# Performance work log

Hardware: AMD Instinct MI355X
Metric: run time of the kernel (lower is better)

The kernel has to match this reference:

```python
import jax, jax.numpy as jnp
import numpy as np

N_NODES = 50000
DEG = 16           # constant out-degree per center node
CUTOFF = 5.0


def setup_inputs() -> dict:
    key = jax.random.key(0)
    k1, k2 = jax.random.split(key)
    # positions scaled so a meaningful fraction of edges exceed the cutoff
    pos = jax.random.normal(k1, (N_NODES, 3), dtype=jnp.float32) * 3.0
    row = jnp.repeat(jnp.arange(N_NODES, dtype=jnp.int32), DEG)      # [E]
    col = jax.random.randint(k2, (N_NODES * DEG,), 0, N_NODES, dtype=jnp.int32)
    edge_index = jnp.stack([row, col], axis=0)                        # [2, E]
    return {"pos": pos, "edge_index": edge_index}


def reference(pos, edge_index):
    """Padded, vectorized DimeNet-style triplet generation.

    Assumes constant degree: edge_index[0] == repeat(arange(N), DEG), so the
    neighbor list of node i is edge_index[1].reshape(N, DEG)[i]. Triplets are
    the [N, DEG, DEG] all-pairs grid; `mask` marks entries that the original
    Python-loop implementation would actually emit (both edges within cutoff,
    j-slot != k-slot).  Masked slots carry 0 for angles/distances.
    """
    num_nodes = pos.shape[0]
    deg = edge_index.shape[1] // num_nodes
    nb = edge_index[1].reshape(num_nodes, deg)          # [N, d] neighbor ids

    R1 = pos[nb] - pos[:, None, :]                      # [N, d, 3] i -> neighbor vectors
    edge_dist = jnp.linalg.norm(R1, axis=-1)            # [N, d]
    valid = edge_dist <= CUTOFF                         # cutoff filter per edge

    diag = jnp.eye(deg, dtype=bool)
    mask = valid[:, :, None] & valid[:, None, :] & ~diag  # [N, d, d]

    # angle(j, i, k) = atan2(|R1_j x R1_k|, R1_j . R1_k)
    dot = jnp.einsum('njc,nkc->njk', R1, R1)            # [N, d, d]
    cross = jnp.cross(R1[:, :, None, :], R1[:, None, :, :])  # [N, d, d, 3]
    cn2 = jnp.sum(cross * cross, axis=-1)
    cross_norm = jnp.sqrt(jnp.where(mask, cn2, 1.0))    # safe sqrt on padded slots
    angles = jnp.where(mask, jnp.arctan2(cross_norm, dot), 0.0)

    # |pos_j - pos_k| = |R1_j - R1_k|
    dvec = R1[:, :, None, :] - R1[:, None, :, :]
    d2 = jnp.sum(dvec * dvec, axis=-1)
    distances_jk = jnp.where(mask, jnp.sqrt(jnp.where(mask & (d2 > 0), d2, 1.0)), 0.0)

    shape3 = (num_nodes, deg, deg)
    id3_i = jnp.broadcast_to(jnp.arange(num_nodes, dtype=jnp.int32)[:, None, None], shape3).reshape(-1)
    id3_j = jnp.broadcast_to(nb[:, :, None], shape3).reshape(-1)
    id3_k = jnp.broadcast_to(nb[:, None, :], shape3).reshape(-1)

    return (id3_i, id3_j, id3_k,
            distances_jk.reshape(-1), angles.reshape(-1), mask.reshape(-1))
```

## Files before the change

kernel.cpp:

```cpp
#include <hip/hip_runtime.h>


#define DEG 16
#define NODES_PER_BLOCK 16
#define THREADS (NODES_PER_BLOCK * 64)
#define CUTOFF_F 5.0f

typedef float f32x4 __attribute__((ext_vector_type(4)));

__device__ __forceinline__ float fast_atan2_pos(float y, float x) {
    const float PI_F   = 3.14159274f;
    const float PIO2_F = 1.57079637f;
    const float ax = fabsf(x);
    const float mn = fminf(ax, y);
    const float mx = fmaxf(ax, y);
    const float a = (mx > 0.0f) ? __fdividef(mn, mx) : 0.0f;
    const float s = a * a;
    float r = fmaf(s, fmaf(s, fmaf(s, fmaf(s, 0.0208351f, -0.085133f),
                                   0.180141f), -0.3302995f), 0.9998660f);
    r *= a;
    if (y > ax)    r = PIO2_F - r;
    if (x < 0.0f)  r = PI_F - r;
    return r;
}

__global__ __launch_bounds__(THREADS) void triplet_kernel(
    const float* __restrict__ pos,
    const int* __restrict__ col_idx,
    float* __restrict__ out,
    int num_nodes, int P)
{
    __shared__ float sx[THREADS / 4], sy[THREADS / 4], sz[THREADS / 4];
    __shared__ float scolf[THREADS / 4];
    __shared__ int   sval[THREADS / 4];

    const int base = blockIdx.x * NODES_PER_BLOCK;
    const int tid = threadIdx.x;

    if (tid < NODES_PER_BLOCK * DEG) {
        int nl = tid >> 4;
        int slot = tid & 15;
        int node = base + nl;
        if (node < num_nodes) {
            int c = col_idx[node * DEG + slot];
            float px = pos[3 * node], py = pos[3 * node + 1], pz = pos[3 * node + 2];
            float rx = pos[3 * c]     - px;
            float ry = pos[3 * c + 1] - py;
            float rz = pos[3 * c + 2] - pz;
            float d = sqrtf(rx * rx + ry * ry + rz * rz);
            sx[tid] = rx; sy[tid] = ry; sz[tid] = rz;
            scolf[tid] = (float)c;
            sval[tid] = (d <= CUTOFF_F) ? 1 : 0;
        }
    }
    __syncthreads();

    const int w = tid >> 6;
    const int lane = tid & 63;
    const int node = base + w;
    if (node >= num_nodes) return;

    const int ofs = w * DEG;
    const int j = lane >> 2;
    const int k0 = (lane & 3) << 2;

    const float jx = sx[ofs + j], jy = sy[ofs + j], jz = sz[ofs + j];
    const int   jv = sval[ofs + j];
    const float jcolf = scolf[ofs + j];

    f32x4 o_k, o_d, o_a, o_m;

    #pragma unroll
    for (int q = 0; q < 4; ++q) {
        const int k = k0 + q;
        const float kx = sx[ofs + k], ky = sy[ofs + k], kz = sz[ofs + k];
        const int   kv = sval[ofs + k];
        const bool m = (jv != 0) && (kv != 0) && (j != k);

        const float dot = jx * kx + jy * ky + jz * kz;
        const float cx = jy * kz - jz * ky;
        const float cy = jz * kx - jx * kz;
        const float cz = jx * ky - jy * kx;
        const float cn2 = cx * cx + cy * cy + cz * cz;
        const float ang = m ? fast_atan2_pos(sqrtf(cn2), dot) : 0.0f;

        const float dx = jx - kx, dy = jy - ky, dz = jz - kz;
        const float d2 = dx * dx + dy * dy + dz * dz;
        const float dist = m ? sqrtf(d2 > 0.0f ? d2 : 1.0f) : 0.0f;

        o_k[q] = scolf[ofs + k];
        o_d[q] = dist;
        o_a[q] = ang;
        o_m[q] = m ? 1.0f : 0.0f;
    }

    const int idx = node * (DEG * DEG) + lane * 4;
    const float fi = (float)node;
    f32x4 o_i; o_i[0] = fi; o_i[1] = fi; o_i[2] = fi; o_i[3] = fi;
    f32x4 o_j; o_j[0] = jcolf; o_j[1] = jcolf; o_j[2] = jcolf; o_j[3] = jcolf;

    float* o0 = out + idx;
    *reinterpret_cast<f32x4*>(o0)         = o_i;
    *reinterpret_cast<f32x4*>(o0 + P)     = o_j;
    *reinterpret_cast<f32x4*>(o0 + 2 * P) = o_k;
    *reinterpret_cast<f32x4*>(o0 + 3 * P) = o_d;
    *reinterpret_cast<f32x4*>(o0 + 4 * P) = o_a;
    *reinterpret_cast<f32x4*>(o0 + 5 * P) = o_m;
}

extern "C" void kernel_launch(void* const* d_in, const int* in_sizes, int n_in,
                              void* d_out, int out_size, void* d_ws, size_t ws_size,
                              hipStream_t stream) {
    const float* pos = (const float*)d_in[0];
    const int* edge_index = (const int*)d_in[1];

    const int num_nodes = in_sizes[0] / 3;
    const int E = in_sizes[1] / 2;
    const int* col = edge_index + E;

    const int P = num_nodes * (DEG * DEG);
    const int blocks = (num_nodes + NODES_PER_BLOCK - 1) / NODES_PER_BLOCK;

    triplet_kernel<<<blocks, THREADS, 0, stream>>>(
        pos, col, (float*)d_out, num_nodes, P);
}
```

Measured before the change: 53.34 us.

## Process two node batches per block, prefetching second batch gathers during first compute

Each block now handles two groups of 16 nodes. The column indices and position gathers for the second group are issued before the first group's triplet compute and stores, so their latency can overlap that work. The second group is then staged into its own shared buffer behind a manual waitcnt and barrier. This halves the grid size and adds register and shared-memory pressure, while the kernel stays dominated by its large output writes.

Result: no change. 53.83 us (+0.9%).

```diff
diff --git a/kernel.cpp b/kernel.cpp
--- a/kernel.cpp
+++ b/kernel.cpp
@@ -2,8 +2,8 @@
 
 
 #define DEG 16
-#define NODES_PER_BLOCK 16
-#define THREADS (NODES_PER_BLOCK * 64)
+#define NPB 16
+#define THREADS (NPB * 64)
 #define CUTOFF_F 5.0f
 
 typedef float f32x4 __attribute__((ext_vector_type(4)));
@@ -24,40 +24,13 @@
     return r;
 }
 
-__global__ __launch_bounds__(THREADS) void triplet_kernel(
-    const float* __restrict__ pos,
-    const int* __restrict__ col_idx,
-    float* __restrict__ out,
-    int num_nodes, int P)
+__device__ __forceinline__ void compute_store(
+    const float* __restrict__ sx, const float* __restrict__ sy,
+    const float* __restrict__ sz, const float* __restrict__ scolf,
+    const int* __restrict__ sval,
+    int node, int num_nodes, int w, int lane,
+    float* __restrict__ out, int P)
 {
-    __shared__ float sx[THREADS / 4], sy[THREADS / 4], sz[THREADS / 4];
-    __shared__ float scolf[THREADS / 4];
-    __shared__ int   sval[THREADS / 4];
-
-    const int base = blockIdx.x * NODES_PER_BLOCK;
-    const int tid = threadIdx.x;
-
-    if (tid < NODES_PER_BLOCK * DEG) {
-        int nl = tid >> 4;
-        int slot = tid & 15;
-        int node = base + nl;
-        if (node < num_nodes) {
-            int c = col_idx[node * DEG + slot];
-            float px = pos[3 * node], py = pos[3 * node + 1], pz = pos[3 * node + 2];
-            float rx = pos[3 * c]     - px;
-            float ry = pos[3 * c + 1] - py;
-            float rz = pos[3 * c + 2] - pz;
-            float d = sqrtf(rx * rx + ry * ry + rz * rz);
-            sx[tid] = rx; sy[tid] = ry; sz[tid] = rz;
-            scolf[tid] = (float)c;
-            sval[tid] = (d <= CUTOFF_F) ? 1 : 0;
-        }
-    }
-    __syncthreads();
-
-    const int w = tid >> 6;
-    const int lane = tid & 63;
-    const int node = base + w;
     if (node >= num_nodes) return;
 
     const int ofs = w * DEG;
@@ -108,6 +81,68 @@
     *reinterpret_cast<f32x4*>(o0 + 5 * P) = o_m;
 }
 
+__global__ __launch_bounds__(THREADS) void triplet_kernel(
+    const float* __restrict__ pos,
+    const int* __restrict__ col_idx,
+    float* __restrict__ out,
+    int num_nodes, int P)
+{
+    __shared__ float sx[2][256], sy[2][256], sz[2][256], scolf[2][256];
+    __shared__ int   sval[2][256];
+
+    const int tid = threadIdx.x;
+    const int w = tid >> 6;
+    const int lane = tid & 63;
+    const int baseA = blockIdx.x * (2 * NPB);
+    const int baseB = baseA + NPB;
+
+    const int nl = tid >> 4;
+    const int slot = tid & 15;
+    const bool stager = (tid < 256);
+    const int nodeB = baseB + nl;
+    const bool haveB = stager && (nodeB < num_nodes);
+
+    int cB = 0;
+    if (haveB) cB = col_idx[nodeB * DEG + slot];
+
+    if (stager) {
+        const int nodeA = baseA + nl;
+        if (nodeA < num_nodes) {
+            const int c = col_idx[nodeA * DEG + slot];
+            const float px = pos[3 * nodeA], py = pos[3 * nodeA + 1], pz = pos[3 * nodeA + 2];
+            const float rx = pos[3 * c]     - px;
+            const float ry = pos[3 * c + 1] - py;
+            const float rz = pos[3 * c + 2] - pz;
+            const float d = sqrtf(rx * rx + ry * ry + rz * rz);
+            sx[0][tid] = rx; sy[0][tid] = ry; sz[0][tid] = rz;
+            scolf[0][tid] = (float)c;
+            sval[0][tid] = (d <= CUTOFF_F) ? 1 : 0;
+        }
+    }
+    __syncthreads();
+
+    float pxB, pyB, pzB, nxB, nyB, nzB;
+    if (haveB) {
+        pxB = pos[3 * nodeB]; pyB = pos[3 * nodeB + 1]; pzB = pos[3 * nodeB + 2];
+        nxB = pos[3 * cB];    nyB = pos[3 * cB + 1];    nzB = pos[3 * cB + 2];
+    }
+
+    compute_store(&sx[0][0], &sy[0][0], &sz[0][0], &scolf[0][0], &sval[0][0],
+                  baseA + w, num_nodes, w, lane, out, P);
+
+    if (haveB) {
+        const float rx = nxB - pxB, ry = nyB - pyB, rz = nzB - pzB;
+        const float d = sqrtf(rx * rx + ry * ry + rz * rz);
+        sx[1][tid] = rx; sy[1][tid] = ry; sz[1][tid] = rz;
+        scolf[1][tid] = (float)cB;
+        sval[1][tid] = (d <= CUTOFF_F) ? 1 : 0;
+    }
+    asm volatile("s_waitcnt lgkmcnt(0)\n\ts_barrier" ::: "memory");
+
+    compute_store(&sx[1][0], &sy[1][0], &sz[1][0], &scolf[1][0], &sval[1][0],
+                  baseB + w, num_nodes, w, lane, out, P);
+}
+
 extern "C" void kernel_launch(void* const* d_in, const int* in_sizes, int n_in,
                               void* d_out, int out_size, void* d_ws, size_t ws_size,
                               hipStream_t stream) {
@@ -119,7 +154,7 @@
     const int* col = edge_index + E;
 
     const int P = num_nodes * (DEG * DEG);
-    const int blocks = (num_nodes + NODES_PER_BLOCK - 1) / NODES_PER_BLOCK;
+    const int blocks = (num_nodes + 2 * NPB - 1) / (2 * NPB);
 
     triplet_kernel<<<blocks, THREADS, 0, stream>>>(
         pos, col, (float*)d_out, num_nodes, P);
```
